# Optimization experiments

Hardware: AMD Instinct MI355X
Metric: run time of the kernel (lower is better)

Reference implementation:

```python
import jax, jax.numpy as jnp
import numpy as np

H = 4096      # number of hyperedges in the batch
N = 20000     # number of unique member nodes
FIN = 256     # in_features
FOUT = 128    # out_features
DEG = 32      # member nodes per hyperedge -> E = H*DEG incidence pairs


def setup_inputs() -> dict:
    key = jax.random.key(0)
    k1, k2, k3, k4 = jax.random.split(key, 4)
    xavier = 1.414 * np.sqrt(2.0 / (FIN + FOUT))  # gain=1.414 xavier scale
    hedge_embed = jax.random.normal(k1, (H, FIN), jnp.float32)
    node_embed = jax.random.normal(k2, (N, FIN), jnp.float32)
    Wq = jax.random.normal(k3, (FIN, FOUT), jnp.float32) * xavier
    # each hyperedge has exactly DEG member nodes (guarantees no empty softmax row)
    row_idx = jnp.repeat(jnp.arange(H, dtype=jnp.int64), DEG)
    col_idx = jax.random.randint(k4, (H * DEG,), 0, N, dtype=jnp.int64)
    return {"hedge_embed": hedge_embed, "node_embed": node_embed, "Wq": Wq,
            "row_idx": row_idx, "col_idx": col_idx}


def reference(hedge_embed, node_embed, Wq, row_idx, col_idx):
    # Faithful to NodeAttAggregator.compute:
    #   - queries AND keys both use query_weight (value_weight is unused in output)
    #   - mask filled with float64-min (overflows to -inf in fp32), member
    #     positions overwritten by scores, then row softmax
    #   - aggregation multiplies attention with the KEY projections
    q = hedge_embed @ Wq                                  # [H, FOUT]
    k = node_embed @ Wq                                   # [N, FOUT]
    scores = (q @ k.T) / jnp.sqrt(jnp.float32(FOUT))      # [H, N]
    member = jnp.zeros((H, N), dtype=bool).at[row_idx, col_idx].set(True)
    masked = jnp.where(member, scores, -jnp.inf)          # non-members -> -inf
    attn = jax.nn.softmax(masked, axis=1)                 # [H, N]
    out = (attn @ k).T                                    # [FOUT, H]
    return out
```

## Files before the change

### kernel.cpp

```cpp
#include <hip/hip_runtime.h>
#include <hip/hip_bf16.h>
#include <stdint.h>

#define H_EDGES 4096
#define N_NODES 20000
#define FIN 256
#define FOUT 128
#define DEG 32
#define ROWS_TOTAL 24096
#define G1_BLOCKS 377

typedef float f32x4 __attribute__((ext_vector_type(4)));
typedef short s16x8 __attribute__((ext_vector_type(8)));
typedef unsigned short u16;

__device__ __forceinline__ u16 f2bf(float f) {
    return __builtin_bit_cast(u16, __float2bfloat16(f));
}
__device__ __forceinline__ float bf2f(u16 h) {
    unsigned u = ((unsigned)h) << 16;
    return __builtin_bit_cast(float, u);
}

__global__ __launch_bounds__(256)
void k0_prep(const float* __restrict__ Wq, u16* __restrict__ bt) {
    __shared__ u16 lt[32][72];
    const int t  = threadIdx.x;
    const int kt = blockIdx.x >> 2;
    const int ct = blockIdx.x & 3;
    const int k0 = kt * 64, c0 = ct * 32;

    #pragma unroll
    for (int p = 0; p < 2; ++p) {
        const int r = p * 32 + (t >> 3);
        const int q = t & 7;
        f32x4 v = *(const f32x4*)(Wq + (size_t)(k0 + r) * FOUT + c0 + q * 4);
        #pragma unroll
        for (int j = 0; j < 4; ++j) lt[q * 4 + j][r] = f2bf(v[j]);
    }
    __syncthreads();

    const int cl = t >> 3;
    const int sl = t & 7;
    const int col = c0 + cl;
    const int s_glob = kt * 8 + sl;
    const int phys = s_glob ^ (col & 7);
    *(s16x8*)(bt + (size_t)(col * 32 + phys) * 8) = *(const s16x8*)&lt[cl][sl * 8];
}

__global__ __launch_bounds__(256)
void g1_gemm(const float* __restrict__ hedge, const float* __restrict__ node,
             const u16* __restrict__ bt, float* __restrict__ qf,
             u16* __restrict__ kb) {
    __shared__ u16 blds[FOUT * FIN];
    const int t = threadIdx.x;
    const int w = t >> 6, l = t & 63;
    const int lr = l & 15, lp = l >> 4;
    const long rb  = (long)blockIdx.x * 64 + w * 16;
    const long row = rb + lr;
    const long arow = row < ROWS_TOTAL ? row : ROWS_TOTAL - 1;
    const float* pa = arow < H_EDGES ? hedge + arow * FIN
                                     : node + (arow - H_EDGES) * FIN;

    f32x4 au[8], av[8];
    #pragma unroll
    for (int ks = 0; ks < 8; ++ks) {
        au[ks] = *(const f32x4*)(pa + ks * 32 + lp * 8);
        av[ks] = *(const f32x4*)(pa + ks * 32 + lp * 8 + 4);
    }

    {
        const s16x8* src = (const s16x8*)bt;
        s16x8* dst = (s16x8*)blds;
        #pragma unroll
        for (int j = 0; j < 16; ++j) { const int s = t + 256 * j; dst[s] = src[s]; }
    }
    __syncthreads();

    f32x4 acc[8];
    #pragma unroll
    for (int j = 0; j < 8; ++j) acc[j] = (f32x4){0.f, 0.f, 0.f, 0.f};

    #pragma unroll
    for (int ks = 0; ks < 8; ++ks) {
        s16x8 a;
        #pragma unroll
        for (int j = 0; j < 4; ++j) {
            a[j]     = (short)f2bf(au[ks][j]);
            a[j + 4] = (short)f2bf(av[ks][j]);
        }
        #pragma unroll
        for (int cf = 0; cf < 8; ++cf) {
            const int col = cf * 16 + lr;
            s16x8 b = *(const s16x8*)(blds +
                (size_t)(col * 32 + ((ks * 4 + lp) ^ (col & 7))) * 8);
            acc[cf] = __builtin_amdgcn_mfma_f32_16x16x32_bf16(a, b, acc[cf], 0, 0, 0);
        }
    }

    if (rb < H_EDGES) {
        #pragma unroll
        for (int i = 0; i < 4; ++i) {
            const long gr = rb + lp * 4 + i;
            #pragma unroll
            for (int cf = 0; cf < 8; ++cf)
                qf[gr * FOUT + cf * 16 + lr] = acc[cf][i];
        }
    } else {
        #pragma unroll
        for (int i = 0; i < 4; ++i) {
            const long gr = rb + lp * 4 + i;
            if (gr < ROWS_TOTAL) {
                #pragma unroll
                for (int cf = 0; cf < 8; ++cf)
                    kb[(gr - H_EDGES) * FOUT + cf * 16 + lr] = f2bf(acc[cf][i]);
            }
        }
    }
}

__global__ __launch_bounds__(256)
void g2_attn(const float* __restrict__ qf, const u16* __restrict__ kb,
             const int* __restrict__ col_idx, float* __restrict__ out) {
    __shared__ __align__(16) char smem[37888];
    const int t = threadIdx.x;
    const int w = t >> 6, l = t & 63;
    const int e = blockIdx.x * 4 + w;

    float (*tile)[4] = (float(*)[4])smem;
    char* base = smem + 2048 + w * 8960;
    u16*   kl  = (u16*)base;
    float* q_l = (float*)(base + 8192);
    float* w_l = q_l + 128;
    int*   c_l = (int*)(w_l + 32);

    if (l < DEG) c_l[l] = col_idx[(size_t)e * DEG + l];
    q_l[l]      = qf[(size_t)e * FOUT + l];
    q_l[l + 64] = qf[(size_t)e * FOUT + 64 + l];

    #pragma unroll
    for (int it = 0; it < 8; ++it) {
        const int s = l + 64 * it;
        const int m = s >> 4, sl = s & 15;
        const int phys = m * 16 + (sl & 8) + ((sl & 7) ^ (m & 7));
        *(s16x8*)(kl + (size_t)phys * 8) =
            *(const s16x8*)(kb + (size_t)c_l[m] * FOUT + sl * 8);
    }

    const int m = l >> 1, he = l & 1;
    float p = 0.f;
    #pragma unroll
    for (int j = 0; j < 8; ++j) {
        const int phys = m * 16 + he * 8 + (j ^ (m & 7));
        s16x8 kv = *(const s16x8*)(kl + (size_t)phys * 8);
        #pragma unroll
        for (int ee = 0; ee < 8; ++ee)
            p = fmaf(q_l[he * 64 + j * 8 + ee], bf2f((u16)kv[ee]), p);
    }
    p += __shfl_xor(p, 1);
    const float sc = p * 0.08838834764831845f;

    const int cm = c_l[m];
    int dup = 0;
    const int jb = he * 16;
    #pragma unroll
    for (int jj = 0; jj < 16; ++jj) {
        const int j = jb + jj;
        dup |= (j < m && c_l[j] == cm) ? 1 : 0;
    }
    dup |= __shfl_xor(dup, 1);

    const float ex = dup ? 0.f : __expf(sc);
    float sum = ex;
    #pragma unroll
    for (int d = 1; d < 64; d <<= 1) sum += __shfl_xor(sum, d);
    const float wgt = ex * 2.f / sum;
    if (he == 0) w_l[m] = wgt;

    float a0 = 0.f, a1 = 0.f;
    const int f0 = 2 * l;
    const int slq = f0 >> 3, eq = f0 & 7;
    #pragma unroll
    for (int mm = 0; mm < DEG; ++mm) {
        const float wv = w_l[mm];
        const int phys = mm * 16 + (slq & 8) + ((slq & 7) ^ (mm & 7));
        const unsigned pv = *(const unsigned*)(kl + (size_t)phys * 8 + eq);
        a0 = fmaf(wv, __builtin_bit_cast(float, pv << 16), a0);
        a1 = fmaf(wv, __builtin_bit_cast(float, pv & 0xFFFF0000u), a1);
    }

    tile[f0][w]     = a0;
    tile[f0 + 1][w] = a1;
    __syncthreads();
    if (t < FOUT) {
        f32x4 v = *(const f32x4*)tile[t];
        *(f32x4*)(out + (size_t)t * H_EDGES + blockIdx.x * 4) = v;
    }
}

extern "C" void kernel_launch(void* const* d_in, const int* in_sizes, int n_in,
                              void* d_out, int out_size, void* d_ws, size_t ws_size,
                              hipStream_t stream) {
    const float* hedge   = (const float*)d_in[0];
    const float* node    = (const float*)d_in[1];
    const float* Wq      = (const float*)d_in[2];
    const int*   col_idx = (const int*)d_in[4];
    float* out = (float*)d_out;

    char* ws = (char*)d_ws;
    float* qf = (float*)ws;
    u16*   kb = (u16*)(ws + (size_t)H_EDGES * FOUT * 4);
    u16*   bt = (u16*)(ws + (size_t)H_EDGES * FOUT * 4
                          + (size_t)N_NODES * FOUT * 2);

    k0_prep<<<16, 256, 0, stream>>>(Wq, bt);
    g1_gemm<<<G1_BLOCKS, 256, 0, stream>>>(hedge, node, bt, qf, kb);
    g2_attn<<<H_EDGES / 4, 256, 0, stream>>>(qf, kb, col_idx, out);
}
```

Measured before the change: 31.91 us.

## Fuse Wq prep into GEMM, add input-touch blocks, split attention across two waves

Removes the separate Wq transpose/convert kernel: each GEMM block now reads fp32 Wq, converts it to bf16 and writes the swizzled layout straight into LDS. Extra 'touch' blocks stream-read all hedge/node rows and discard the result, apparently to warm the cache for the GEMM blocks. The attention kernel moves to 512 threads, so each hyperedge gets two waves that split the gather, scoring and aggregation, with extra barriers between phases. This saves one launch and spreads per-edge work over more waves, at the cost of redundant Wq conversion in every block and roughly doubled input read traffic.

```diff
diff --git a/kernel.cpp b/kernel.cpp
--- a/kernel.cpp
+++ b/kernel.cpp
@@ -8,7 +8,8 @@
 #define FOUT 128
 #define DEG 32
 #define ROWS_TOTAL 24096
-#define G1_BLOCKS 377
+#define G1_GEMM 377
+#define G1_TOUCH 1506
 
 typedef float f32x4 __attribute__((ext_vector_type(4)));
 typedef short s16x8 __attribute__((ext_vector_type(8)));
@@ -23,40 +24,31 @@
 }
 
 __global__ __launch_bounds__(256)
-void k0_prep(const float* __restrict__ Wq, u16* __restrict__ bt) {
-    __shared__ u16 lt[32][72];
-    const int t  = threadIdx.x;
-    const int kt = blockIdx.x >> 2;
-    const int ct = blockIdx.x & 3;
-    const int k0 = kt * 64, c0 = ct * 32;
-
-    #pragma unroll
-    for (int p = 0; p < 2; ++p) {
-        const int r = p * 32 + (t >> 3);
-        const int q = t & 7;
-        f32x4 v = *(const f32x4*)(Wq + (size_t)(k0 + r) * FOUT + c0 + q * 4);
-        #pragma unroll
-        for (int j = 0; j < 4; ++j) lt[q * 4 + j][r] = f2bf(v[j]);
-    }
-    __syncthreads();
-
-    const int cl = t >> 3;
-    const int sl = t & 7;
-    const int col = c0 + cl;
-    const int s_glob = kt * 8 + sl;
-    const int phys = s_glob ^ (col & 7);
-    *(s16x8*)(bt + (size_t)(col * 32 + phys) * 8) = *(const s16x8*)&lt[cl][sl * 8];
-}
-
-__global__ __launch_bounds__(256)
-void g1_gemm(const float* __restrict__ hedge, const float* __restrict__ node,
-             const u16* __restrict__ bt, float* __restrict__ qf,
-             u16* __restrict__ kb) {
+void g1_fused(const float* __restrict__ hedge, const float* __restrict__ node,
+              const float* __restrict__ Wq, float* __restrict__ qf,
+              u16* __restrict__ kb) {
     __shared__ u16 blds[FOUT * FIN];
+    const int bid = blockIdx.x;
     const int t = threadIdx.x;
+
+    if (bid >= G1_GEMM) {
+        const long base = (long)(bid - G1_GEMM) * 1024 + t;
+        float s = 0.f;
+        #pragma unroll
+        for (int j = 0; j < 4; ++j) {
+            const long idx = base + j * 256;
+            const f32x4* p = idx < 262144 ? (const f32x4*)hedge + idx
+                                          : (const f32x4*)node + (idx - 262144);
+            f32x4 v = *p;
+            s += v[0] + v[1] + v[2] + v[3];
+        }
+        asm volatile("" :: "v"(s));
+        return;
+    }
+
     const int w = t >> 6, l = t & 63;
     const int lr = l & 15, lp = l >> 4;
-    const long rb  = (long)blockIdx.x * 64 + w * 16;
+    const long rb  = (long)bid * 64 + w * 16;
     const long row = rb + lr;
     const long arow = row < ROWS_TOTAL ? row : ROWS_TOTAL - 1;
     const float* pa = arow < H_EDGES ? hedge + arow * FIN
@@ -70,10 +62,20 @@
     }
 
     {
-        const s16x8* src = (const s16x8*)bt;
-        s16x8* dst = (s16x8*)blds;
-        #pragma unroll
-        for (int j = 0; j < 16; ++j) { const int s = t + 256 * j; dst[s] = src[s]; }
+        char* bb = (char*)blds;
+        #pragma unroll
+        for (int it = 0; it < 16; ++it) {
+            const int k0 = it * 16 + (t >> 5) * 2;
+            const int c4 = (t & 31) * 4;
+            f32x4 v0 = *(const f32x4*)(Wq + (size_t)k0 * FOUT + c4);
+            f32x4 v1 = *(const f32x4*)(Wq + (size_t)(k0 + 1) * FOUT + c4);
+            #pragma unroll
+            for (int j = 0; j < 4; ++j) {
+                const int col = c4 + j;
+                const unsigned pack = (unsigned)f2bf(v0[j]) | ((unsigned)f2bf(v1[j]) << 16);
+                *(unsigned*)(bb + col * 512 + (((k0 >> 3) ^ (col & 7)) * 16) + (k0 & 7) * 2) = pack;
+            }
+        }
     }
     __syncthreads();
 
@@ -119,79 +121,91 @@
     }
 }
 
-__global__ __launch_bounds__(256)
+__global__ __launch_bounds__(512)
 void g2_attn(const float* __restrict__ qf, const u16* __restrict__ kb,
              const int* __restrict__ col_idx, float* __restrict__ out) {
-    __shared__ __align__(16) char smem[37888];
+    __shared__ __align__(16) char smem[38400];
     const int t = threadIdx.x;
     const int w = t >> 6, l = t & 63;
-    const int e = blockIdx.x * 4 + w;
-
-    float (*tile)[4] = (float(*)[4])smem;
-    char* base = smem + 2048 + w * 8960;
+    const int ei = w >> 1, wv = w & 1;
+    const int e = blockIdx.x * 4 + ei;
+
+    char* base = smem + ei * 9088;
     u16*   kl  = (u16*)base;
     float* q_l = (float*)(base + 8192);
-    float* w_l = q_l + 128;
-    int*   c_l = (int*)(w_l + 32);
-
-    if (l < DEG) c_l[l] = col_idx[(size_t)e * DEG + l];
-    q_l[l]      = qf[(size_t)e * FOUT + l];
-    q_l[l + 64] = qf[(size_t)e * FOUT + 64 + l];
-
-    #pragma unroll
-    for (int it = 0; it < 8; ++it) {
+    float* s_l = (float*)(base + 8704);
+    float* w_l = (float*)(base + 8832);
+    int*   c_l = (int*)(base + 8960);
+    float (*tile)[4] = (float(*)[4])(smem + 36352);
+
+    if (l < 16) c_l[wv * 16 + l] = col_idx[(size_t)e * DEG + wv * 16 + l];
+    q_l[wv * 64 + l] = qf[(size_t)e * FOUT + wv * 64 + l];
+    #pragma unroll
+    for (int it = 0; it < 4; ++it) {
         const int s = l + 64 * it;
-        const int m = s >> 4, sl = s & 15;
+        const int m = wv * 16 + (s >> 4), sl = s & 15;
         const int phys = m * 16 + (sl & 8) + ((sl & 7) ^ (m & 7));
         *(s16x8*)(kl + (size_t)phys * 8) =
             *(const s16x8*)(kb + (size_t)c_l[m] * FOUT + sl * 8);
     }
-
-    const int m = l >> 1, he = l & 1;
-    float p = 0.f;
-    #pragma unroll
-    for (int j = 0; j < 8; ++j) {
-        const int phys = m * 16 + he * 8 + (j ^ (m & 7));
-        s16x8 kv = *(const s16x8*)(kl + (size_t)phys * 8);
-        #pragma unroll
-        for (int ee = 0; ee < 8; ++ee)
-            p = fmaf(q_l[he * 64 + j * 8 + ee], bf2f((u16)kv[ee]), p);
-    }
-    p += __shfl_xor(p, 1);
-    const float sc = p * 0.08838834764831845f;
-
-    const int cm = c_l[m];
-    int dup = 0;
-    const int jb = he * 16;
-    #pragma unroll
-    for (int jj = 0; jj < 16; ++jj) {
-        const int j = jb + jj;
-        dup |= (j < m && c_l[j] == cm) ? 1 : 0;
-    }
-    dup |= __shfl_xor(dup, 1);
-
-    const float ex = dup ? 0.f : __expf(sc);
-    float sum = ex;
-    #pragma unroll
-    for (int d = 1; d < 64; d <<= 1) sum += __shfl_xor(sum, d);
-    const float wgt = ex * 2.f / sum;
-    if (he == 0) w_l[m] = wgt;
-
-    float a0 = 0.f, a1 = 0.f;
-    const int f0 = 2 * l;
-    const int slq = f0 >> 3, eq = f0 & 7;
-    #pragma unroll
-    for (int mm = 0; mm < DEG; ++mm) {
-        const float wv = w_l[mm];
-        const int phys = mm * 16 + (slq & 8) + ((slq & 7) ^ (mm & 7));
-        const unsigned pv = *(const unsigned*)(kl + (size_t)phys * 8 + eq);
-        a0 = fmaf(wv, __builtin_bit_cast(float, pv << 16), a0);
-        a1 = fmaf(wv, __builtin_bit_cast(float, pv & 0xFFFF0000u), a1);
-    }
-
-    tile[f0][w]     = a0;
-    tile[f0 + 1][w] = a1;
-    __syncthreads();
+    __syncthreads();
+
+    {
+        const int m = wv * 16 + (l >> 2);
+        const int qq = l & 3;
+        float p = 0.f;
+        #pragma unroll
+        for (int j = 0; j < 4; ++j) {
+            const int sl = qq * 4 + j;
+            const int phys = m * 16 + (sl & 8) + ((sl & 7) ^ (m & 7));
+            s16x8 kv = *(const s16x8*)(kl + (size_t)phys * 8);
+            const int e0 = qq * 32 + j * 8;
+            f32x4 qa = *(const f32x4*)&q_l[e0];
+            f32x4 qb = *(const f32x4*)&q_l[e0 + 4];
+            #pragma unroll
+            for (int ee = 0; ee < 4; ++ee) {
+                p = fmaf(qa[ee], bf2f((u16)kv[ee]), p);
+                p = fmaf(qb[ee], bf2f((u16)kv[ee + 4]), p);
+            }
+        }
+        p += __shfl_xor(p, 1);
+        p += __shfl_xor(p, 2);
+        if (qq == 0) s_l[m] = p * 0.08838834764831845f;
+    }
+    __syncthreads();
+
+    {
+        const int m2 = l >> 1, he = l & 1;
+        const int cm = c_l[m2];
+        const float sv = s_l[m2];
+        int dup = 0;
+        const int jb = he * 16;
+        #pragma unroll
+        for (int jj = 0; jj < 16; ++jj) {
+            const int j = jb + jj;
+            dup |= (j < m2 && c_l[j] == cm) ? 1 : 0;
+        }
+        dup |= __shfl_xor(dup, 1);
+        const float ex = dup ? 0.f : __expf(sv);
+        float sum = ex;
+        #pragma unroll
+        for (int d = 1; d < 64; d <<= 1) sum += __shfl_xor(sum, d);
+        if (he == 0) w_l[m2] = ex * 2.f / sum;
+    }
+
+    {
+        const int f = wv * 64 + l;
+        const int sl0 = f >> 3, el = f & 7;
+        float a = 0.f;
+        #pragma unroll
+        for (int mm = 0; mm < DEG; ++mm) {
+            const int phys = mm * 16 + (sl0 & 8) + ((sl0 & 7) ^ (mm & 7));
+            a = fmaf(w_l[mm], bf2f(kl[(size_t)phys * 8 + el]), a);
+        }
+        tile[f][ei] = a;
+    }
+    __syncthreads();
+
     if (t < FOUT) {
         f32x4 v = *(const f32x4*)tile[t];
         *(f32x4*)(out + (size_t)t * H_EDGES + blockIdx.x * 4) = v;
@@ -210,10 +224,7 @@
     char* ws = (char*)d_ws;
     float* qf = (float*)ws;
     u16*   kb = (u16*)(ws + (size_t)H_EDGES * FOUT * 4);
-    u16*   bt = (u16*)(ws + (size_t)H_EDGES * FOUT * 4
-                          + (size_t)N_NODES * FOUT * 2);
-
-    k0_prep<<<16, 256, 0, stream>>>(Wq, bt);
-    g1_gemm<<<G1_BLOCKS, 256, 0, stream>>>(hedge, node, bt, qf, kb);
-    g2_attn<<<H_EDGES / 4, 256, 0, stream>>>(qf, kb, col_idx, out);
-}
+
+    g1_fused<<<G1_GEMM + G1_TOUCH, 256, 0, stream>>>(hedge, node, Wq, qf, kb);
+    g2_attn<<<H_EDGES / 4, 512, 0, stream>>>(qf, kb, col_idx, out);
+}
```

Measured after the change: 31.33 us. No clear change (-1.8%).
